# Optimization experiments

Measured on AMD Instinct MI355X. Metric: run time of the kernel, lower is better.

The kernel has to match this reference:

```python
import jax, jax.numpy as jnp
import numpy as np

D_MODEL = 1024
NUM_HEADS = 16
HEAD_DIM = D_MODEL // NUM_HEADS


def setup_inputs() -> dict:
    key = jax.random.key(0)
    k1, k2, k3 = jax.random.split(key, 3)
    B, S = 2, 2048
    x = jax.random.normal(k1, (B, S, D_MODEL), dtype=jnp.float32)
    # torch nn.Linear weight layout: [out_features, in_features]
    qkv_w = jax.random.normal(k2, (3 * D_MODEL, D_MODEL), dtype=jnp.float32) * (D_MODEL ** -0.5)
    qkv_b = jnp.zeros((3 * D_MODEL,), dtype=jnp.float32)
    out_w = jax.random.normal(k3, (D_MODEL, D_MODEL), dtype=jnp.float32) * (D_MODEL ** -0.5)
    out_b = jnp.zeros((D_MODEL,), dtype=jnp.float32)
    return {"x": x, "qkv_w": qkv_w, "qkv_b": qkv_b, "out_w": out_w, "out_b": out_b}


def reference(x, qkv_w, qkv_b, out_w, out_b):
    B, S, D = x.shape
    H, hd = NUM_HEADS, HEAD_DIM
    # fused QKV projection (torch Linear: x @ W.T + b)
    qkv = jnp.dot(x, qkv_w.T) + qkv_b              # [B, S, 3D]
    qkv = qkv.reshape(B, S, 3, H, hd)
    qkv = jnp.transpose(qkv, (2, 0, 3, 1, 4))       # [3, B, H, S, hd]
    q, k, v = qkv[0], qkv[1], qkv[2]
    scale = hd ** -0.5
    scores = jnp.einsum('bhqd,bhkd->bhqk', q, k) * scale  # [B, H, S, S]
    # causal mask (TritonSoftmax(is_causal=True))
    causal = jnp.tril(jnp.ones((S, S), dtype=bool))
    scores = jnp.where(causal, scores, jnp.float32(-jnp.inf))
    attn = jax.nn.softmax(scores, axis=-1)
    ctx = jnp.einsum('bhqk,bhkd->bhqd', attn, v)    # [B, H, S, hd]
    ctx = jnp.transpose(ctx, (0, 2, 1, 3)).reshape(B, S, D)
    return jnp.dot(ctx, out_w.T) + out_b
```

## Files before the change

kernel.cpp:

```cpp
#include <hip/hip_runtime.h>

typedef unsigned short u16;
typedef __bf16 bf16x8 __attribute__((ext_vector_type(8)));
typedef float f32x4 __attribute__((ext_vector_type(4)));
typedef float f32x16 __attribute__((ext_vector_type(16)));
typedef unsigned u32x2v __attribute__((ext_vector_type(2)));

#define LOG2E 1.44269504088896340736f

__device__ __forceinline__ u16 f2bf(float f) {
  unsigned int u = __builtin_bit_cast(unsigned int, f);
  u += 0x7FFFu + ((u >> 16) & 1u);
  return (u16)(u >> 16);
}

__device__ __forceinline__ unsigned pack2(float lo, float hi) {
  return (unsigned)f2bf(lo) | ((unsigned)f2bf(hi) << 16);
}

__device__ __forceinline__ void pl32swap(unsigned& a, unsigned& b) {
  u32x2v r = __builtin_amdgcn_permlane32_swap(a, b, false, false);
  a = r[0]; b = r[1];
}

__device__ __forceinline__ void async16(const void* g, void* l) {
  __builtin_amdgcn_global_load_lds((void*)g, (void*)l, 16, 0, 0);
}

__global__ void cast_all(const float* __restrict__ x, const float* __restrict__ w1,
                         const float* __restrict__ w2, u16* __restrict__ xb,
                         u16* __restrict__ w1b, u16* __restrict__ w2b) {
  int i = blockIdx.x * blockDim.x + threadIdx.x;
  const float* s; u16* d; int j;
  if (i < 1048576)      { s = x;  d = xb;  j = i; }
  else if (i < 1835008) { s = w1; d = w1b; j = i - 1048576; }
  else                  { s = w2; d = w2b; j = i - 1835008; }
  float4 v = ((const float4*)s)[j];
  union { u16 s4[4]; uint2 u; } o;
  o.s4[0] = f2bf(v.x); o.s4[1] = f2bf(v.y); o.s4[2] = f2bf(v.z); o.s4[3] = f2bf(v.w);
  ((uint2*)d)[j] = o.u;
}

template <int EPI, int BN>
__global__ __launch_bounds__(256)
void gemm_nt(const u16* __restrict__ A, const u16* __restrict__ Bw,
             int M, int N, int K, const float* __restrict__ bias,
             u16* __restrict__ qo, u16* __restrict__ ko, u16* __restrict__ vto,
             float* __restrict__ out, int ntn) {
  __shared__ __align__(16) u16 As[128 * 32];
  __shared__ __align__(16) u16 Bs[BN * 32];
  constexpr int JN = BN / 32;
  constexpr int NB = (BN * 4) / 256;
  const int tid = threadIdx.x;
  const int w = tid >> 6, lane = tid & 63;
  const int lr = lane & 15, lkb = lane >> 4;
  const int bx = blockIdx.x;
  const int mt = bx / ntn, nt = bx % ntn;
  const int m0 = mt * 128, n0 = nt * BN;
  const int wm = (w >> 1) * 64, wn = (w & 1) * (BN / 2);

  f32x4 acc[4][JN] = {};

  int srow[2], sgch[2];
#pragma unroll
  for (int i = 0; i < 2; ++i) {
    int cid = tid + i * 256;
    srow[i] = cid >> 2;
    sgch[i] = (cid & 3) ^ (srow[i] & 3);
  }

  for (int k0 = 0; k0 < K; k0 += 32) {
#pragma unroll
    for (int i = 0; i < 2; ++i) {
      char* la = (char*)As + (w * 64 + i * 256) * 16;
      async16(A + (size_t)(m0 + srow[i]) * K + k0 + sgch[i] * 8, la);
    }
#pragma unroll
    for (int i = 0; i < NB; ++i) {
      char* lb = (char*)Bs + (w * 64 + i * 256) * 16;
      async16(Bw + (size_t)(n0 + srow[i]) * K + k0 + sgch[i] * 8, lb);
    }
    __syncthreads();

    bf16x8 af[4], bfr[JN];
#pragma unroll
    for (int i = 0; i < 4; ++i) {
      int ra = wm + i * 16 + lr;
      af[i] = *(const bf16x8*)(As + ra * 32 + (lkb ^ (ra & 3)) * 8);
    }
#pragma unroll
    for (int j = 0; j < JN; ++j) {
      int rb = wn + j * 16 + lr;
      bfr[j] = *(const bf16x8*)(Bs + rb * 32 + (lkb ^ (rb & 3)) * 8);
    }
#pragma unroll
    for (int i = 0; i < 4; ++i)
#pragma unroll
      for (int j = 0; j < JN; ++j)
        acc[i][j] = __builtin_amdgcn_mfma_f32_16x16x32_bf16(af[i], bfr[j], acc[i][j], 0, 0, 0);
    __syncthreads();
  }

  if constexpr (EPI == 0) {
    const int which = n0 >> 10;
    const float qscale = (which == 0) ? 0.125f : 1.0f;
#pragma unroll
    for (int i = 0; i < 4; ++i) {
#pragma unroll
      for (int j = 0; j < JN; ++j) {
        int n = n0 + wn + j * 16 + lr;
        float bv = bias[n];
        int d = n & 1023, h = d >> 6, dd = d & 63;
#pragma unroll
        for (int r = 0; r < 4; ++r) {
          int m = m0 + wm + i * 16 + lkb * 4 + r;
          int b = m >> 11, s = m & 2047;
          int bh = b * 16 + h;
          u16 val = f2bf((acc[i][j][r] + bv) * qscale);
          if (which == 0)      qo[(bh * 2048 + s) * 64 + dd] = val;
          else if (which == 1) ko[(bh * 2048 + s) * 64 + dd] = val;
          else                 vto[(bh * 64 + dd) * 2048 + s] = val;
        }
      }
    }
  } else {
#pragma unroll
    for (int i = 0; i < 4; ++i)
#pragma unroll
      for (int j = 0; j < JN; ++j) {
        int n = n0 + wn + j * 16 + lr;
        float bv = bias[n];
#pragma unroll
        for (int r = 0; r < 4; ++r) {
          int m = m0 + wm + i * 16 + lkb * 4 + r;
          out[(size_t)m * N + n] = acc[i][j][r] + bv;
        }
      }
  }
}

__global__ __launch_bounds__(256, 2)
void flash_attn(const u16* __restrict__ Q, const u16* __restrict__ Kg,
                const u16* __restrict__ Vt, u16* __restrict__ ctx) {
  __shared__ __align__(16) u16 Kls[2][64 * 64];
  __shared__ __align__(16) u16 Vls[2][64 * 64];
  const int tid = threadIdx.x;
  const int w = tid >> 6, lane = tid & 63;
  const int l5 = lane & 31, hi = lane >> 5;
  const int bid = blockIdx.x;
  const int h = bid & 31;
  const int tt = bid >> 5;
  const int qt = (tt < 8) ? (15 - tt) : (tt - 8);
  const int q0w = qt * 128 + w * 32;
  const int qrow = q0w + l5;
  const u16* Qh = Q + (size_t)h * 2048 * 64;
  const u16* Kh = Kg + (size_t)h * 2048 * 64;
  const u16* Vh = Vt + (size_t)h * 2048 * 64;

  bf16x8 bQ[4];
#pragma unroll
  for (int ks = 0; ks < 4; ++ks)
    bQ[ks] = *(const bf16x8*)(Qh + (size_t)qrow * 64 + ks * 16 + hi * 8);

  f32x16 accO[2] = {};
  float m_r = -1e30f, l_r = 0.f;

  const int ra = tid & 63, ca = tid >> 6;
  const int cb = ca + 4;
  char* const ldA_K0 = (char*)&Kls[0][0] + (w * 64) * 16;
  char* const ldB_K0 = (char*)&Kls[0][0] + (w * 64 + 256) * 16;
  char* const ldA_V0 = (char*)&Vls[0][0] + (w * 64) * 16;
  char* const ldB_V0 = (char*)&Vls[0][0] + (w * 64 + 256) * 16;
  const int bufstep = 64 * 64 * 2;

  const int nkv = 2 * qt + 2;

  async16(Kh + (size_t)ra * 64 + ca * 8, ldA_K0);
  async16(Kh + (size_t)ra * 64 + cb * 8, ldB_K0);
  async16(Vh + (size_t)ra * 2048 + ca * 8, ldA_V0);
  async16(Vh + (size_t)ra * 2048 + cb * 8, ldB_V0);
  __syncthreads();

  for (int t = 0; t < nkv; ++t) {
    const int cur = t & 1;
    const int kv0 = t * 64;
    if (t + 1 < nkv) {
      const int kv1 = kv0 + 64;
      const int bo = (cur ^ 1) * bufstep;
      async16(Kh + (size_t)(kv1 + ra) * 64 + ca * 8, ldA_K0 + bo);
      async16(Kh + (size_t)(kv1 + ra) * 64 + cb * 8, ldB_K0 + bo);
      async16(Vh + (size_t)ra * 2048 + kv1 + ca * 8, ldA_V0 + bo);
      async16(Vh + (size_t)ra * 2048 + kv1 + cb * 8, ldB_V0 + bo);
    }
    if (kv0 <= q0w + 31) {
      const u16* Kb = &Kls[cur][0];
      const u16* Vb = &Vls[cur][0];

      f32x16 sg[2];
      __builtin_amdgcn_s_setprio(1);
#pragma unroll
      for (int g = 0; g < 2; ++g) {
        f32x16 z = {};
#pragma unroll
        for (int ks = 0; ks < 4; ++ks) {
          bf16x8 ka = *(const bf16x8*)(Kb + ((ks * 2 + hi) * 64 + g * 32 + l5) * 8);
          z = __builtin_amdgcn_mfma_f32_32x32x16_bf16(ka, bQ[ks], z, 0, 0, 0);
        }
        sg[g] = z;
      }
      __builtin_amdgcn_s_setprio(0);

      if (kv0 + 63 > q0w) {
#pragma unroll
        for (int g = 0; g < 2; ++g)
#pragma unroll
          for (int r = 0; r < 16; ++r) {
            int kv = kv0 + g * 32 + (r & 3) + 8 * (r >> 2) + 4 * hi;
            if (kv > qrow) sg[g][r] = -1e30f;
          }
      }

      float mt = sg[0][0];
#pragma unroll
      for (int r = 1; r < 16; ++r) mt = fmaxf(mt, sg[0][r]);
#pragma unroll
      for (int r = 0; r < 16; ++r) mt = fmaxf(mt, sg[1][r]);
      {
        unsigned a = __builtin_bit_cast(unsigned, mt), b = a;
        pl32swap(a, b);
        mt = fmaxf(__builtin_bit_cast(float, a), __builtin_bit_cast(float, b));
      }

      if (!__all(mt <= m_r + 8.0f)) {
        float mnew = fmaxf(m_r, mt);
        float sca = exp2f((m_r - mnew) * LOG2E);
        l_r *= sca;
        accO[0] *= sca;
        accO[1] *= sca;
        m_r = mnew;
      }
      const float mls = m_r * LOG2E;
      float rs = 0.f;
#pragma unroll
      for (int g = 0; g < 2; ++g)
#pragma unroll
        for (int r = 0; r < 16; ++r) {
          float p = exp2f(__builtin_fmaf(sg[g][r], LOG2E, -mls));
          sg[g][r] = p;
          rs += p;
        }
      {
        unsigned a = __builtin_bit_cast(unsigned, rs), b = a;
        pl32swap(a, b);
        rs = __builtin_bit_cast(float, a) + __builtin_bit_cast(float, b);
      }
      l_r += rs;

      bf16x8 Pf[4];
#pragma unroll
      for (int s = 0; s < 4; ++s) {
        const int g = s >> 1, b8 = (s & 1) * 8;
        unsigned w0 = pack2(sg[g][b8 + 0], sg[g][b8 + 1]);
        unsigned w1 = pack2(sg[g][b8 + 2], sg[g][b8 + 3]);
        unsigned w2 = pack2(sg[g][b8 + 4], sg[g][b8 + 5]);
        unsigned w3 = pack2(sg[g][b8 + 6], sg[g][b8 + 7]);
        pl32swap(w0, w2);
        pl32swap(w1, w3);
        uint4 bb = {w0, w1, w2, w3};
        Pf[s] = __builtin_bit_cast(bf16x8, bb);
      }

      __builtin_amdgcn_s_setprio(1);
#pragma unroll
      for (int g = 0; g < 2; ++g)
#pragma unroll
        for (int s = 0; s < 4; ++s) {
          bf16x8 va = *(const bf16x8*)(Vb + ((s * 2 + hi) * 64 + g * 32 + l5) * 8);
          accO[g] = __builtin_amdgcn_mfma_f32_32x32x16_bf16(va, Pf[s], accO[g], 0, 0, 0);
        }
      __builtin_amdgcn_s_setprio(0);
    }
    __syncthreads();
  }

  const float rl = 1.0f / l_r;
  const int b = h >> 4, hh = h & 15;
  const size_t base = ((size_t)(b * 2048 + qrow)) * 1024 + hh * 64;
#pragma unroll
  for (int g = 0; g < 2; ++g)
#pragma unroll
    for (int qd = 0; qd < 4; ++qd) {
      uint2 o;
      o.x = pack2(accO[g][qd * 4 + 0] * rl, accO[g][qd * 4 + 1] * rl);
      o.y = pack2(accO[g][qd * 4 + 2] * rl, accO[g][qd * 4 + 3] * rl);
      *(uint2*)(ctx + base + g * 32 + qd * 8 + hi * 4) = o;
    }
}

extern "C" void kernel_launch(void* const* d_in, const int* in_sizes, int n_in,
                              void* d_out, int out_size, void* d_ws, size_t ws_size,
                              hipStream_t stream) {
  (void)in_sizes; (void)n_in; (void)out_size; (void)ws_size;
  const float* x = (const float*)d_in[0];
  const float* qkv_w = (const float*)d_in[1];
  const float* qkv_b = (const float*)d_in[2];
  const float* out_w = (const float*)d_in[3];
  const float* out_b = (const float*)d_in[4];
  float* out = (float*)d_out;

  char* ws = (char*)d_ws;
  u16* xb   = (u16*)(ws);
  u16* wqkv = (u16*)(ws + 8388608);
  u16* wout = (u16*)(ws + 14680064);
  u16* Qb   = (u16*)(ws + 16777216);
  u16* Kb   = (u16*)(ws + 25165824);
  u16* Vtb  = (u16*)(ws + 33554432);
  u16* ctx  = (u16*)(ws + 41943040);

  cast_all<<<8192, 256, 0, stream>>>(x, qkv_w, out_w, xb, wqkv, wout);

  gemm_nt<0, 128><<<768, 256, 0, stream>>>(xb, wqkv, 4096, 3072, 1024, qkv_b,
                                           Qb, Kb, Vtb, nullptr, 24);
  flash_attn<<<512, 256, 0, stream>>>(Qb, Kb, Vtb, ctx);
  gemm_nt<1, 64><<<512, 256, 0, stream>>>(ctx, wout, 4096, 1024, 1024, out_b,
                                          nullptr, nullptr, nullptr, out, 16);
}
```

Measured before the change: 214.0 us.

## Triple-buffer K/V tiles with explicit vmcnt waits and use hardware bf16 pack

Flash attention K/V staging moves from double to triple buffering in LDS. Two tiles are prefetched ahead, and explicit s_waitcnt vmcnt counts plus raw s_barrier replace the __syncthreads-based scheme. This gives global loads more time to land before the tile is used. The software bf16 rounding is replaced with the v_cvt_pk_bf16_f32 instruction, and the row max and row sum reductions become trees to shorten dependency chains. The extra LDS buffer raises shared memory use per block, which may limit occupancy at the 2-blocks launch bound.

```diff
diff --git a/kernel.cpp b/kernel.cpp
--- a/kernel.cpp
+++ b/kernel.cpp
@@ -14,8 +14,10 @@
   return (u16)(u >> 16);
 }
 
-__device__ __forceinline__ unsigned pack2(float lo, float hi) {
-  return (unsigned)f2bf(lo) | ((unsigned)f2bf(hi) << 16);
+__device__ __forceinline__ unsigned cvtpk_bf16(float lo, float hi) {
+  unsigned r;
+  asm("v_cvt_pk_bf16_f32 %0, %1, %2" : "=v"(r) : "v"(lo), "v"(hi));
+  return r;
 }
 
 __device__ __forceinline__ void pl32swap(unsigned& a, unsigned& b) {
@@ -142,8 +144,8 @@
 __global__ __launch_bounds__(256, 2)
 void flash_attn(const u16* __restrict__ Q, const u16* __restrict__ Kg,
                 const u16* __restrict__ Vt, u16* __restrict__ ctx) {
-  __shared__ __align__(16) u16 Kls[2][64 * 64];
-  __shared__ __align__(16) u16 Vls[2][64 * 64];
+  __shared__ __align__(16) u16 Kls[3][64 * 64];
+  __shared__ __align__(16) u16 Vls[3][64 * 64];
   const int tid = threadIdx.x;
   const int w = tid >> 6, lane = tid & 63;
   const int l5 = lane & 31, hi = lane >> 5;
@@ -165,36 +167,41 @@
   f32x16 accO[2] = {};
   float m_r = -1e30f, l_r = 0.f;
 
-  const int ra = tid & 63, ca = tid >> 6;
-  const int cb = ca + 4;
-  char* const ldA_K0 = (char*)&Kls[0][0] + (w * 64) * 16;
-  char* const ldB_K0 = (char*)&Kls[0][0] + (w * 64 + 256) * 16;
-  char* const ldA_V0 = (char*)&Vls[0][0] + (w * 64) * 16;
-  char* const ldB_V0 = (char*)&Vls[0][0] + (w * 64 + 256) * 16;
-  const int bufstep = 64 * 64 * 2;
+  const int ra = tid & 63, ca = tid >> 6, cb = ca + 4;
+  char* const kq = (char*)&Kls[0][0] + w * 1024;
+  char* const vq = (char*)&Vls[0][0] + w * 1024;
+
+#define STAGE(tile, bi) do {                                            \
+    const int _bo = (bi) * 8192;                                        \
+    async16(Kh + (size_t)((tile) * 64 + ra) * 64 + ca * 8, kq + _bo);   \
+    async16(Kh + (size_t)((tile) * 64 + ra) * 64 + cb * 8, kq + _bo + 4096); \
+    async16(Vh + (size_t)ra * 2048 + (tile) * 64 + ca * 8, vq + _bo);   \
+    async16(Vh + (size_t)ra * 2048 + (tile) * 64 + cb * 8, vq + _bo + 4096); \
+  } while (0)
 
   const int nkv = 2 * qt + 2;
-
-  async16(Kh + (size_t)ra * 64 + ca * 8, ldA_K0);
-  async16(Kh + (size_t)ra * 64 + cb * 8, ldB_K0);
-  async16(Vh + (size_t)ra * 2048 + ca * 8, ldA_V0);
-  async16(Vh + (size_t)ra * 2048 + cb * 8, ldB_V0);
-  __syncthreads();
-
+  STAGE(0, 0);
+  STAGE(1, 1);
+
+  int bcur = 0;
   for (int t = 0; t < nkv; ++t) {
-    const int cur = t & 1;
+    const int rem = nkv - t;
+    if (rem > 2) {
+      int b2 = bcur + 2; if (b2 >= 3) b2 -= 3;
+      STAGE(t + 2, b2);
+      asm volatile("s_waitcnt vmcnt(8)" ::: "memory");
+    } else if (rem > 1) {
+      asm volatile("s_waitcnt vmcnt(4)" ::: "memory");
+    } else {
+      asm volatile("s_waitcnt vmcnt(0)" ::: "memory");
+    }
+    __builtin_amdgcn_s_barrier();
+    __builtin_amdgcn_sched_barrier(0);
+
     const int kv0 = t * 64;
-    if (t + 1 < nkv) {
-      const int kv1 = kv0 + 64;
-      const int bo = (cur ^ 1) * bufstep;
-      async16(Kh + (size_t)(kv1 + ra) * 64 + ca * 8, ldA_K0 + bo);
-      async16(Kh + (size_t)(kv1 + ra) * 64 + cb * 8, ldB_K0 + bo);
-      async16(Vh + (size_t)ra * 2048 + kv1 + ca * 8, ldA_V0 + bo);
-      async16(Vh + (size_t)ra * 2048 + kv1 + cb * 8, ldB_V0 + bo);
-    }
     if (kv0 <= q0w + 31) {
-      const u16* Kb = &Kls[cur][0];
-      const u16* Vb = &Vls[cur][0];
+      const u16* Kb = &Kls[bcur][0];
+      const u16* Vb = &Vls[bcur][0];
 
       f32x16 sg[2];
       __builtin_amdgcn_s_setprio(1);
@@ -220,11 +227,13 @@
           }
       }
 
-      float mt = sg[0][0];
-#pragma unroll
-      for (int r = 1; r < 16; ++r) mt = fmaxf(mt, sg[0][r]);
-#pragma unroll
-      for (int r = 0; r < 16; ++r) mt = fmaxf(mt, sg[1][r]);
+      float t8[8];
+#pragma unroll
+      for (int i = 0; i < 8; ++i)
+        t8[i] = fmaxf(fmaxf(sg[0][i], sg[0][i + 8]), fmaxf(sg[1][i], sg[1][i + 8]));
+      float t4a = fmaxf(t8[0], t8[4]), t4b = fmaxf(t8[1], t8[5]);
+      float t4c = fmaxf(t8[2], t8[6]), t4d = fmaxf(t8[3], t8[7]);
+      float mt = fmaxf(fmaxf(t4a, t4b), fmaxf(t4c, t4d));
       {
         unsigned a = __builtin_bit_cast(unsigned, mt), b = a;
         pl32swap(a, b);
@@ -240,15 +249,19 @@
         m_r = mnew;
       }
       const float mls = m_r * LOG2E;
-      float rs = 0.f;
 #pragma unroll
       for (int g = 0; g < 2; ++g)
 #pragma unroll
-        for (int r = 0; r < 16; ++r) {
-          float p = exp2f(__builtin_fmaf(sg[g][r], LOG2E, -mls));
-          sg[g][r] = p;
-          rs += p;
-        }
+        for (int r = 0; r < 16; ++r)
+          sg[g][r] = exp2f(__builtin_fmaf(sg[g][r], LOG2E, -mls));
+
+      float s8[8];
+#pragma unroll
+      for (int i = 0; i < 8; ++i)
+        s8[i] = (sg[0][i] + sg[0][i + 8]) + (sg[1][i] + sg[1][i + 8]);
+      float s4a = s8[0] + s8[4], s4b = s8[1] + s8[5];
+      float s4c = s8[2] + s8[6], s4d = s8[3] + s8[7];
+      float rs = (s4a + s4b) + (s4c + s4d);
       {
         unsigned a = __builtin_bit_cast(unsigned, rs), b = a;
         pl32swap(a, b);
@@ -260,10 +273,10 @@
 #pragma unroll
       for (int s = 0; s < 4; ++s) {
         const int g = s >> 1, b8 = (s & 1) * 8;
-        unsigned w0 = pack2(sg[g][b8 + 0], sg[g][b8 + 1]);
-        unsigned w1 = pack2(sg[g][b8 + 2], sg[g][b8 + 3]);
-        unsigned w2 = pack2(sg[g][b8 + 4], sg[g][b8 + 5]);
-        unsigned w3 = pack2(sg[g][b8 + 6], sg[g][b8 + 7]);
+        unsigned w0 = cvtpk_bf16(sg[g][b8 + 0], sg[g][b8 + 1]);
+        unsigned w1 = cvtpk_bf16(sg[g][b8 + 2], sg[g][b8 + 3]);
+        unsigned w2 = cvtpk_bf16(sg[g][b8 + 4], sg[g][b8 + 5]);
+        unsigned w3 = cvtpk_bf16(sg[g][b8 + 6], sg[g][b8 + 7]);
         pl32swap(w0, w2);
         pl32swap(w1, w3);
         uint4 bb = {w0, w1, w2, w3};
@@ -280,8 +293,10 @@
         }
       __builtin_amdgcn_s_setprio(0);
     }
-    __syncthreads();
+    __builtin_amdgcn_s_barrier();
+    if (++bcur == 3) bcur = 0;
   }
+#undef STAGE
 
   const float rl = 1.0f / l_r;
   const int b = h >> 4, hh = h & 15;
@@ -291,8 +306,8 @@
 #pragma unroll
     for (int qd = 0; qd < 4; ++qd) {
       uint2 o;
-      o.x = pack2(accO[g][qd * 4 + 0] * rl, accO[g][qd * 4 + 1] * rl);
-      o.y = pack2(accO[g][qd * 4 + 2] * rl, accO[g][qd * 4 + 3] * rl);
+      o.x = cvtpk_bf16(accO[g][qd * 4 + 0] * rl, accO[g][qd * 4 + 1] * rl);
+      o.y = cvtpk_bf16(accO[g][qd * 4 + 2] * rl, accO[g][qd * 4 + 3] * rl);
       *(uint2*)(ctx + base + g * 32 + qd * 8 + hi * 4) = o;
     }
 }
```

After: 211.9 us. No clear change (-1.0%).
